# Optimization experiments

Hardware: AMD Instinct MI355X
Metric: run time of the kernel (lower is better)

The kernel has to match this reference:

```python
import jax, jax.numpy as jnp
import numpy as np

N, P, K, DIMS = 32, 1024, 16, 3
C_IN, C_MID, C_OUT, DM = 64, 64, 128, 2


def setup_inputs() -> dict:
    key = jax.random.key(0)
    ks = jax.random.split(key, 12)
    s = 0.05
    return {
        "rep_pt": jax.random.normal(ks[0], (N, P, DIMS), jnp.float32),
        "pts": jax.random.normal(ks[1], (N, P, K, DIMS), jnp.float32),
        "fts": jax.random.normal(ks[2], (N, P, K, C_IN), jnp.float32),
        # dense1 / dense2 (Linear + ELU)
        "w1": jax.random.normal(ks[3], (DIMS, C_MID), jnp.float32) * s,
        "b1": jnp.zeros((C_MID,), jnp.float32),
        "w2": jax.random.normal(ks[4], (C_MID, C_MID), jnp.float32) * s,
        "b2": jnp.zeros((C_MID,), jnp.float32),
        # conv2d: Conv2d(dims, K*K, (1,K)) -> weight (K*K, dims, K) (kernel h=1 squeezed)
        "wconv": jax.random.normal(ks[5], (K * K, DIMS, K), jnp.float32) * s,
        "bconv": jnp.zeros((K * K,), jnp.float32),
        # depthwise Conv2d(K, K*K, (1,K), groups=K) -> weight (K,K,K) [group i, mult j, tap k]
        "wdep1": jax.random.normal(ks[6], (K, K, K), jnp.float32) * s,
        "bdep1": jnp.zeros((K, K), jnp.float32),
        "wdep2": jax.random.normal(ks[7], (K, K, K), jnp.float32) * s,
        "bdep2": jnp.zeros((K, K), jnp.float32),
        # SepConv: depthwise Conv2d(C, C*DM, (1,K), groups=C) + pointwise Conv2d(C*DM, C_out, 1)
        "wdw": jax.random.normal(ks[8], (C_MID + C_IN, DM, K), jnp.float32) * s,
        "bdw": jnp.zeros((C_MID + C_IN, DM), jnp.float32),
        "wpw": jax.random.normal(ks[9], (C_OUT, C_MID + C_IN, DM), jnp.float32) * s,
        "bpw": jnp.zeros((C_OUT,), jnp.float32),
    }


def reference(rep_pt, pts, fts, w1, b1, w2, b2, wconv, bconv,
              wdep1, bdep1, wdep2, bdep2, wdw, bdw, wpw, bpw):
    n, p, k, _ = pts.shape
    # localize neighbors around representative point
    pts_local = pts - rep_pt[:, :, None, :]                      # (N,P,K,dims)
    # lift point coords to C_mid features (two Linear+ELU)
    h = jax.nn.elu(pts_local @ w1 + b1)
    h = jax.nn.elu(h @ w2 + b2)                                  # (N,P,K,C_mid)
    fts_cat = jnp.concatenate([h, fts], axis=-1)                 # (N,P,K,C_mid+C_in)
    # Conv2d(dims -> K*K, kernel (1,K)): full contraction over neighbor axis k
    X = jax.nn.elu(jnp.einsum('npkc,ock->npo', pts_local, wconv) + bconv)
    X = X.reshape(n, p, k, k)                                    # (N,P,K,K)
    # depthwise convs, groups=K, depth_multiplier=K, kernel (1,K):
    # channels-last input channel is last K axis (i), conv taps run over third axis (k)
    X = jax.nn.elu(jnp.einsum('npki,ijk->npij', X, wdep1) + bdep1)
    X = jnp.einsum('npki,ijk->npij', X, wdep2) + bdep2           # (N,P,K,K), no activation
    # learned X-transform applied to features
    fts_X = jnp.einsum('npkj,npjc->npkc', X, fts_cat)            # (N,P,K,C_mid+C_in)
    # separable conv over neighbor axis: depthwise (1,K) then pointwise 1x1
    tmp = jnp.einsum('npkc,cmk->npcm', fts_X, wdw) + bdw         # (N,P,C,DM)
    out = jax.nn.elu(jnp.einsum('npcm,ocm->npo', tmp, wpw) + bpw)
    return out                                                   # (N,P,C_out)
```

## Files before the change

kernel.cpp:

```cpp
#include <hip/hip_runtime.h>
#include <hip/hip_bf16.h>


#define ELU(x) ((x) > 0.0f ? (x) : (__expf(x) - 1.0f))

__device__ __forceinline__ void lds_fence() {
    asm volatile("s_waitcnt lgkmcnt(0)" ::: "memory");
}

typedef __attribute__((ext_vector_type(8))) short short8v;
typedef __attribute__((ext_vector_type(4))) float f32x4;
#define MFMA32(a, b, c) __builtin_amdgcn_mfma_f32_16x16x32_bf16(a, b, c, 0, 0, 0)

__device__ __forceinline__ short f2bf(float x) {
    __hip_bfloat16 h = __float2bfloat16(x);
    return *reinterpret_cast<short*>(&h);
}
__device__ __forceinline__ float bf2f(short x) {
    unsigned u = ((unsigned)(unsigned short)x) << 16;
    return __uint_as_float(u);
}
__device__ __forceinline__ void gload_lds16(const float* g, float* l) {
    __builtin_amdgcn_global_load_lds(
        (const __attribute__((address_space(1))) void*)g,
        (__attribute__((address_space(3))) void*)l,
        16, 0, 0);
}

#define XW_WC   0
#define XW_WD1  8192
#define XW_WD2  12352
#define XW_BC   16512
#define XW_BD1  16768
#define XW_BD2  17024
#define XW_SCR  17280
#define XW_TOTAL (17280 + 4*4368)

__global__ __launch_bounds__(256) void k_xform(
    const float* __restrict__ rep, const float* __restrict__ pts,
    const float* __restrict__ wconv, const float* __restrict__ bconv,
    const float* __restrict__ wdep1, const float* __restrict__ bdep1,
    const float* __restrict__ wdep2, const float* __restrict__ bdep2,
    float* __restrict__ x2)
{
    extern __shared__ __align__(16) float sm[];
    short* smh = (short*)sm;
    const int tid = threadIdx.x;

    for (int e = tid; e < 2048; e += 256) {
        const int part = e >> 10, u = (e >> 6) & 15, l = e & 63;
        const int g = l >> 4, s = l & 15;
        const int o = u * 16 + s;
        short8v v;
        if (part == 0) {
            #pragma unroll
            for (int t = 0; t < 8; ++t) v[t] = f2bf(wconv[o*48 + g*8 + t]);
        } else {
            #pragma unroll
            for (int t = 0; t < 4; ++t) v[t] = f2bf(wconv[o*48 + 32 + g*4 + t]);
            #pragma unroll
            for (int t = 4; t < 8; ++t) v[t] = 0;
        }
        *(short8v*)&smh[e * 8] = v;
    }
    for (int e = tid; e < 4096; e += 256) {
        const int i = e >> 8, j = (e >> 4) & 15, k = e & 15;
        sm[XW_WD1 + i*260 + j*16 + k] = wdep1[e];
        sm[XW_WD2 + i*260 + j*16 + k] = wdep2[e];
    }
    sm[XW_BC  + tid] = bconv[tid];
    sm[XW_BD1 + tid] = bdep1[tid];
    sm[XW_BD2 + tid] = bdep2[tid];
    __syncthreads();

    const int wave = tid >> 6, lane = tid & 63;
    const int g = lane >> 4, s = lane & 15;
    const int pt0 = (blockIdx.x * 4 + wave) * 16;

    const int p = pt0 + s;
    const float r0 = rep[p*3], r1 = rep[p*3+1], r2 = rep[p*3+2];
    short8v ah0, al0, ah1, al1;
    #pragma unroll
    for (int e = 0; e < 8; ++e) {
        const int r = g*8 + e;
        const int d = g >> 1, k = r & 15;
        const float v = pts[p*48 + k*3 + d] - (d == 0 ? r0 : r1);
        const short h = f2bf(v);
        ah0[e] = h; al0[e] = f2bf(v - bf2f(h));
    }
    #pragma unroll
    for (int e = 0; e < 4; ++e) {
        const int k = g*4 + e;
        const float v = pts[p*48 + k*3 + 2] - r2;
        const short h = f2bf(v);
        ah1[e] = h; al1[e] = f2bf(v - bf2f(h));
    }
    #pragma unroll
    for (int e = 4; e < 8; ++e) { ah1[e] = 0; al1[e] = 0; }

    f32x4 ex[16];
    #pragma unroll
    for (int u = 0; u < 16; ++u) {
        const float b = sm[XW_BC + u*16 + s];
        f32x4 acc; acc[0] = b; acc[1] = b; acc[2] = b; acc[3] = b;
        const short8v bh0 = *(const short8v*)&smh[(u*64 + lane) * 8];
        const short8v bh1 = *(const short8v*)&smh[((16 + u)*64 + lane) * 8];
        acc = MFMA32(ah0, bh0, acc);
        acc = MFMA32(ah1, bh1, acc);
        acc = MFMA32(al0, bh0, acc);
        acc = MFMA32(al1, bh1, acc);
        f32x4 r;
        r[0] = ELU(acc[0]); r[1] = ELU(acc[1]); r[2] = ELU(acc[2]); r[3] = ELU(acc[3]);
        ex[u] = r;
    }

    const int scrb = XW_SCR + wave * 4368;
    #pragma unroll
    for (int j = 0; j < 16; ++j) {
        const float b = sm[XW_BD1 + s*16 + j];
        f32x4 a; a[0] = b; a[1] = b; a[2] = b; a[3] = b;
        #pragma unroll
        for (int kb = 0; kb < 4; ++kb) {
            const float4 w = *(const float4*)&sm[XW_WD1 + s*260 + j*16 + kb*4];
            a += ex[kb*4+0] * w.x; a += ex[kb*4+1] * w.y;
            a += ex[kb*4+2] * w.z; a += ex[kb*4+3] * w.w;
        }
        #pragma unroll
        for (int q = 0; q < 4; ++q)
            sm[scrb + (g*4+q)*273 + j*17 + s] = ELU(a[q]);
    }
    lds_fence();

    f32x4 xr[16];
    #pragma unroll
    for (int k = 0; k < 16; ++k) {
        f32x4 v;
        #pragma unroll
        for (int q = 0; q < 4; ++q)
            v[q] = sm[scrb + (g*4+q)*273 + s*17 + k];
        xr[k] = v;
    }
    f32x4 oj[16];
    #pragma unroll
    for (int j = 0; j < 16; ++j) {
        const float b = sm[XW_BD2 + s*16 + j];
        f32x4 a; a[0] = b; a[1] = b; a[2] = b; a[3] = b;
        #pragma unroll
        for (int kb = 0; kb < 4; ++kb) {
            const float4 w = *(const float4*)&sm[XW_WD2 + s*260 + j*16 + kb*4];
            a += xr[kb*4+0] * w.x; a += xr[kb*4+1] * w.y;
            a += xr[kb*4+2] * w.z; a += xr[kb*4+3] * w.w;
        }
        oj[j] = a;
    }
    #pragma unroll
    for (int q = 0; q < 4; ++q) {
        const int pp = pt0 + g*4 + q;
        #pragma unroll
        for (int jb = 0; jb < 4; ++jb) {
            *(float4*)&x2[pp*256 + s*16 + jb*4] =
                make_float4(oj[jb*4+0][q], oj[jb*4+1][q], oj[jb*4+2][q], oj[jb*4+3][q]);
        }
    }
}

__global__ __launch_bounds__(256, 3) void k_feat(
    const float* __restrict__ rep, const float* __restrict__ pts, const float* __restrict__ fts,
    const float* __restrict__ w1, const float* __restrict__ b1,
    const float* __restrict__ w2, const float* __restrict__ b2,
    const float* __restrict__ wdw, const float* __restrict__ bdw,
    float* __restrict__ xbuf)
{
    __shared__ __align__(16) short sw2[4096];
    __shared__ __align__(16) uint2 sw1[64];
    __shared__ __align__(16) unsigned swdwp[2560];
    __shared__ float sbdw[256];
    __shared__ __align__(16) float sfts[4][2][1024];
    const int tid = threadIdx.x;

    for (int idx = tid; idx < 512; idx += 256) {
        const int r = idx >> 6, l = idx & 63;
        const int nt = r >> 1, h = r & 1, gg = l >> 4, ss = l & 15;
        short8v v;
        #pragma unroll
        for (int e = 0; e < 8; ++e)
            v[e] = f2bf(w2[(h*32 + gg*8 + e)*64 + nt*16 + ss]);
        *(short8v*)&sw2[idx * 8] = v;
    }
    if (tid < 64) {
        const int j = tid;
        uint2 v;
        v.x = (unsigned)(unsigned short)f2bf(w1[j])
            | (((unsigned)(unsigned short)f2bf(w1[64 + j])) << 16);
        v.y = (unsigned)(unsigned short)f2bf(w1[128 + j])
            | (((unsigned)(unsigned short)f2bf(b1[j])) << 16);
        sw1[j] = v;
    }
    for (int e = tid; e < 2048; e += 256) {
        const int m = e >> 10, c = (e >> 3) & 127, w = e & 7;
        const unsigned lo = (unsigned)(unsigned short)f2bf(wdw[c*32 + m*16 + 2*w]);
        const unsigned hi = (unsigned)(unsigned short)f2bf(wdw[c*32 + m*16 + 2*w + 1]);
        swdwp[m*1280 + c*10 + w] = lo | (hi << 16);
    }
    sbdw[tid] = bdw[tid];
    __syncthreads();

    const int lane = tid & 63, wave = tid >> 6;
    const int g = lane >> 4, s = lane & 15;

    float b2c[4];
    #pragma unroll
    for (int nt = 0; nt < 4; ++nt) b2c[nt] = b2[nt*16 + s];

    const int pt0 = (blockIdx.x * 4 + wave) * 8;
    float* sf0 = &sfts[wave][0][0];
    float* sf1 = &sfts[wave][1][0];

    {
        const float* src = fts + (size_t)pt0 * 1024 + lane * 4;
        #pragma unroll
        for (int i = 0; i < 4; ++i) gload_lds16(src + i*256, sf0 + i*256);
    }

    for (int it = 0; it < 8; ++it) {
        const int pt = pt0 + it;
        float* sfc = (it & 1) ? sf1 : sf0;
        float* sfn = (it & 1) ? sf0 : sf1;

        const float4 xv = *(const float4*)&xbuf[(size_t)pt*256 + s*16 + g*4];
        const float p0 = pts[pt*48 + s*3 + 0] - rep[pt*3 + 0];
        const float p1 = pts[pt*48 + s*3 + 1] - rep[pt*3 + 1];
        const float p2 = pts[pt*48 + s*3 + 2] - rep[pt*3 + 2];

        if (it < 7) {
            const float* src = fts + (size_t)(pt + 1) * 1024 + lane * 4;
            #pragma unroll
            for (int i = 0; i < 4; ++i) gload_lds16(src + i*256, sfn + i*256);
        }

        short8v af0, af1;
        #pragma unroll
        for (int t = 0; t < 2; ++t) {
            short8v f;
            #pragma unroll
            for (int e = 0; e < 8; ++e) {
                const uint2 pk = sw1[t*32 + g*8 + e];
                const float wx = __uint_as_float(pk.x << 16);
                const float wy = __uint_as_float(pk.x & 0xffff0000u);
                const float wz = __uint_as_float(pk.y << 16);
                const float bb = __uint_as_float(pk.y & 0xffff0000u);
                float h = bb + p0*wx + p1*wy + p2*wz;
                h = ELU(h);
                f[e] = f2bf(h);
            }
            if (t == 0) af0 = f; else af1 = f;
        }
        f32x4 hacc[4];
        #pragma unroll
        for (int nt = 0; nt < 4; ++nt) {
            f32x4 a; a[0] = b2c[nt]; a[1] = b2c[nt]; a[2] = b2c[nt]; a[3] = b2c[nt];
            const short8v bf0 = *(const short8v*)&sw2[((nt*2 + 0)*64 + lane) * 8];
            const short8v bf1 = *(const short8v*)&sw2[((nt*2 + 1)*64 + lane) * 8];
            a = MFMA32(af0, bf0, a);
            a = MFMA32(af1, bf1, a);
            hacc[nt] = a;
        }
        short8v a2 = (short8v)0;
        a2[0] = f2bf(xv.x); a2[1] = f2bf(xv.y);
        a2[2] = f2bf(xv.z); a2[3] = f2bf(xv.w);

        asm volatile("s_waitcnt vmcnt(4)" ::: "memory");

        #pragma unroll
        for (int u = 0; u < 8; ++u) {
            short8v bfrag = (short8v)0;
            if (u < 4) {
                #pragma unroll
                for (int q = 0; q < 4; ++q) bfrag[q] = f2bf(ELU(hacc[u][q]));
            } else {
                #pragma unroll
                for (int e = 0; e < 4; ++e)
                    bfrag[e] = f2bf(sfc[(g*4 + e)*64 + (u - 4)*16 + s]);
            }
            f32x4 z; z[0] = 0.f; z[1] = 0.f; z[2] = 0.f; z[3] = 0.f;
            const f32x4 fx = MFMA32(a2, bfrag, z);

            const int c = u*16 + s;
            const int wo = c*10 + 2*g;
            const uint2 wm0 = *(const uint2*)&swdwp[wo];
            const uint2 wm1 = *(const uint2*)&swdwp[1280 + wo];
            const float a0 = __uint_as_float(wm0.x << 16);
            const float a1 = __uint_as_float(wm0.x & 0xffff0000u);
            const float a2f = __uint_as_float(wm0.y << 16);
            const float a3 = __uint_as_float(wm0.y & 0xffff0000u);
            const float c0 = __uint_as_float(wm1.x << 16);
            const float c1 = __uint_as_float(wm1.x & 0xffff0000u);
            const float c2 = __uint_as_float(wm1.y << 16);
            const float c3 = __uint_as_float(wm1.y & 0xffff0000u);
            float q0 = fx[0]*a0 + fx[1]*a1 + fx[2]*a2f + fx[3]*a3;
            float q1 = fx[0]*c0 + fx[1]*c1 + fx[2]*c2 + fx[3]*c3;
            q0 += __shfl_xor(q0, 16); q0 += __shfl_xor(q0, 32);
            q1 += __shfl_xor(q1, 16); q1 += __shfl_xor(q1, 32);
            if (lane < 16) {
                float2 r; r.x = q0 + sbdw[2*c]; r.y = q1 + sbdw[2*c + 1];
                *(float2*)&xbuf[(size_t)pt*256 + 2*c] = r;
            }
        }
    }
}

__global__ __launch_bounds__(256) void k_out(
    const float* __restrict__ tmp, const float* __restrict__ wpw,
    const float* __restrict__ bpw, float* __restrict__ out)
{
    __shared__ unsigned sb[16384];
    const int tid = threadIdx.x;
    for (int e = tid; e < 16384; e += 256) {
        const int n = e >> 7, kw = e & 127;
        const int cb = kw >> 2, wi = kw & 3;
        const unsigned lo = (unsigned)(unsigned short)f2bf(wpw[n*256 + 2*kw]);
        const unsigned hi = (unsigned)(unsigned short)f2bf(wpw[n*256 + 2*kw + 1]);
        sb[n*128 + ((cb ^ (n & 7)) << 2) + wi] = lo | (hi << 16);
    }
    __syncthreads();

    const int lane = tid & 63, wave = tid >> 6;
    const int g = lane >> 4, s = lane & 15;
    const int row = blockIdx.x * 64 + wave * 16 + s;

    f32x4 acc[8];
    #pragma unroll
    for (int nt = 0; nt < 8; ++nt) {
        const float b = bpw[nt*16 + s];
        acc[nt][0] = b; acc[nt][1] = b; acc[nt][2] = b; acc[nt][3] = b;
    }

    const float* arow = tmp + (size_t)row * 256 + g*8;
    float4 pa0 = *(const float4*)(arow);
    float4 pa1 = *(const float4*)(arow + 4);

    #pragma unroll
    for (int kk = 0; kk < 8; ++kk) {
        const float4 a0 = pa0, a1 = pa1;
        if (kk < 7) {
            pa0 = *(const float4*)(arow + (kk+1)*32);
            pa1 = *(const float4*)(arow + (kk+1)*32 + 4);
        }
        short8v ah, al;
        const float av[8] = {a0.x, a0.y, a0.z, a0.w, a1.x, a1.y, a1.z, a1.w};
        #pragma unroll
        for (int e = 0; e < 8; ++e) {
            const short h = f2bf(av[e]);
            ah[e] = h;
            al[e] = f2bf(av[e] - bf2f(h));
        }
        #pragma unroll
        for (int nt = 0; nt < 8; ++nt) {
            const short8v bf = *(const short8v*)&sb[(nt*16 + s)*128 + (((kk*4 + g) ^ (s & 7)) << 2)];
            acc[nt] = MFMA32(ah, bf, acc[nt]);
            acc[nt] = MFMA32(al, bf, acc[nt]);
        }
    }
    const int rbase = blockIdx.x * 64 + wave * 16 + 4*g;
    #pragma unroll
    for (int nt = 0; nt < 8; ++nt)
        #pragma unroll
        for (int q = 0; q < 4; ++q)
            out[(size_t)(rbase + q) * 128 + nt*16 + s] = ELU(acc[nt][q]);
}

extern "C" void kernel_launch(void* const* d_in, const int* in_sizes, int n_in,
                              void* d_out, int out_size, void* d_ws, size_t ws_size,
                              hipStream_t stream)
{
    (void)in_sizes; (void)n_in; (void)out_size; (void)ws_size;
    const float* rep   = (const float*)d_in[0];
    const float* pts   = (const float*)d_in[1];
    const float* fts   = (const float*)d_in[2];
    const float* w1    = (const float*)d_in[3];
    const float* b1    = (const float*)d_in[4];
    const float* w2    = (const float*)d_in[5];
    const float* b2    = (const float*)d_in[6];
    const float* wconv = (const float*)d_in[7];
    const float* bconv = (const float*)d_in[8];
    const float* wdep1 = (const float*)d_in[9];
    const float* bdep1 = (const float*)d_in[10];
    const float* wdep2 = (const float*)d_in[11];
    const float* bdep2 = (const float*)d_in[12];
    const float* wdw   = (const float*)d_in[13];
    const float* bdw   = (const float*)d_in[14];
    const float* wpw   = (const float*)d_in[15];
    const float* bpw   = (const float*)d_in[16];
    float* out  = (float*)d_out;
    float* xbuf = (float*)d_ws;

    hipFuncSetAttribute((const void*)k_xform, hipFuncAttributeMaxDynamicSharedMemorySize, XW_TOTAL*4);

    k_xform<<<dim3(512),  dim3(256), XW_TOTAL*4, stream>>>(rep, pts, wconv, bconv, wdep1, bdep1, wdep2, bdep2, xbuf);
    k_feat <<<dim3(1024), dim3(256), 0, stream>>>(rep, pts, fts, w1, b1, w2, b2, wdw, bdw, xbuf);
    k_out  <<<dim3(512),  dim3(256), 0, stream>>>(xbuf, wpw, bpw, out);
}
```

Measured before the change: 111.5 us.

## Make k_feat persistent with grid-stride points and prefetch per-point inputs

Switches k_feat from 1024 blocks that each process 8 contiguous points per wave to 768 persistent blocks (3 per CU on 256 CUs), where each wave strides over points by the total wave count. It also prefetches the next point's xbuf row and pts/rep coordinates into registers together with the fts LDS prefetch, and adjusts the vmcnt wait to match. The intent is to remove tail effects and one-time weight setup per block, and to hide global load latency. The risk is poorer locality from strided point access and more live registers.

```diff
diff --git a/kernel.cpp b/kernel.cpp
--- a/kernel.cpp
+++ b/kernel.cpp
@@ -164,6 +164,8 @@
     }
 }
 
+#define NPTS 32768
+#define TOTW 3072
 __global__ __launch_bounds__(256, 3) void k_feat(
     const float* __restrict__ rep, const float* __restrict__ pts, const float* __restrict__ fts,
     const float* __restrict__ w1, const float* __restrict__ b1,
@@ -212,30 +214,37 @@
     #pragma unroll
     for (int nt = 0; nt < 4; ++nt) b2c[nt] = b2[nt*16 + s];
 
-    const int pt0 = (blockIdx.x * 4 + wave) * 8;
+    const int gw = blockIdx.x * 4 + wave;
     float* sf0 = &sfts[wave][0][0];
     float* sf1 = &sfts[wave][1][0];
 
     {
-        const float* src = fts + (size_t)pt0 * 1024 + lane * 4;
+        const float* src = fts + (size_t)gw * 1024 + lane * 4;
         #pragma unroll
         for (int i = 0; i < 4; ++i) gload_lds16(src + i*256, sf0 + i*256);
     }
-
-    for (int it = 0; it < 8; ++it) {
-        const int pt = pt0 + it;
-        float* sfc = (it & 1) ? sf1 : sf0;
-        float* sfn = (it & 1) ? sf0 : sf1;
-
-        const float4 xv = *(const float4*)&xbuf[(size_t)pt*256 + s*16 + g*4];
-        const float p0 = pts[pt*48 + s*3 + 0] - rep[pt*3 + 0];
-        const float p1 = pts[pt*48 + s*3 + 1] - rep[pt*3 + 1];
-        const float p2 = pts[pt*48 + s*3 + 2] - rep[pt*3 + 2];
-
-        if (it < 7) {
-            const float* src = fts + (size_t)(pt + 1) * 1024 + lane * 4;
+    float4 xv_n = *(const float4*)&xbuf[(size_t)gw*256 + s*16 + g*4];
+    float p0_n = pts[gw*48 + s*3 + 0] - rep[gw*3 + 0];
+    float p1_n = pts[gw*48 + s*3 + 1] - rep[gw*3 + 1];
+    float p2_n = pts[gw*48 + s*3 + 2] - rep[gw*3 + 2];
+
+    int k = 0;
+    for (int pt = gw; pt < NPTS; pt += TOTW, ++k) {
+        float* sfc = (k & 1) ? sf1 : sf0;
+        float* sfn = (k & 1) ? sf0 : sf1;
+        const int ptn = pt + TOTW;
+
+        const float4 xv = xv_n;
+        const float p0 = p0_n, p1 = p1_n, p2 = p2_n;
+
+        if (ptn < NPTS) {
+            const float* src = fts + (size_t)ptn * 1024 + lane * 4;
             #pragma unroll
             for (int i = 0; i < 4; ++i) gload_lds16(src + i*256, sfn + i*256);
+            xv_n = *(const float4*)&xbuf[(size_t)ptn*256 + s*16 + g*4];
+            p0_n = pts[ptn*48 + s*3 + 0] - rep[ptn*3 + 0];
+            p1_n = pts[ptn*48 + s*3 + 1] - rep[ptn*3 + 1];
+            p2_n = pts[ptn*48 + s*3 + 2] - rep[ptn*3 + 2];
         }
 
         short8v af0, af1;
@@ -269,7 +278,8 @@
         a2[0] = f2bf(xv.x); a2[1] = f2bf(xv.y);
         a2[2] = f2bf(xv.z); a2[3] = f2bf(xv.w);
 
-        asm volatile("s_waitcnt vmcnt(4)" ::: "memory");
+        if (ptn < NPTS) { asm volatile("s_waitcnt vmcnt(8)" ::: "memory"); }
+        else           { asm volatile("s_waitcnt vmcnt(0)" ::: "memory"); }
 
         #pragma unroll
         for (int u = 0; u < 8; ++u) {
@@ -396,7 +406,7 @@
 
     hipFuncSetAttribute((const void*)k_xform, hipFuncAttributeMaxDynamicSharedMemorySize, XW_TOTAL*4);
 
-    k_xform<<<dim3(512),  dim3(256), XW_TOTAL*4, stream>>>(rep, pts, wconv, bconv, wdep1, bdep1, wdep2, bdep2, xbuf);
-    k_feat <<<dim3(1024), dim3(256), 0, stream>>>(rep, pts, fts, w1, b1, w2, b2, wdw, bdw, xbuf);
-    k_out  <<<dim3(512),  dim3(256), 0, stream>>>(xbuf, wpw, bpw, out);
-}
+    k_xform<<<dim3(512), dim3(256), XW_TOTAL*4, stream>>>(rep, pts, wconv, bconv, wdep1, bdep1, wdep2, bdep2, xbuf);
+    k_feat <<<dim3(768), dim3(256), 0, stream>>>(rep, pts, fts, w1, b1, w2, b2, wdw, bdw, xbuf);
+    k_out  <<<dim3(512), dim3(256), 0, stream>>>(xbuf, wpw, bpw, out);
+}
```

Result: faster. 105.4 us (-5.5%).
